# Performance work log

Measured on AMD Instinct MI355X. Metric: run time of the kernel, lower is better.

The kernel has to match this reference:

```python
import jax, jax.numpy as jnp
import numpy as np

N_NODES = 100000
N_EDGES = 3200000
IN_DIM = 128
OUT_DIM = 64
ITERS = 2


def setup_inputs() -> dict:
    key = jax.random.key(0)
    k1, k2, k3, k4, k5, k6 = jax.random.split(key, 6)
    feature = jax.random.normal(k1, (N_NODES, IN_DIM), dtype=jnp.float32)
    src = jax.random.randint(k2, (N_EDGES,), 0, N_NODES, dtype=jnp.int32)
    dst = jax.random.randint(k3, (N_EDGES,), 0, N_NODES, dtype=jnp.int32)
    # Kaiming-ish scaling for stability
    W_lin = jax.random.normal(k4, (IN_DIM, OUT_DIM), dtype=jnp.float32) / np.sqrt(IN_DIM)
    W_d1 = jax.random.normal(k5, (OUT_DIM, OUT_DIM), dtype=jnp.float32) / np.sqrt(OUT_DIM)
    W_d2 = jax.random.normal(k6, (OUT_DIM, OUT_DIM), dtype=jnp.float32) / np.sqrt(OUT_DIM)
    return {"feature": feature, "src": src, "dst": dst,
            "W_lin": W_lin, "W_d1": W_d1, "W_d2": W_d2}


def reference(feature, src, dst, W_lin, W_d1, W_d2):
    # u_i^0 = 0 ; u_i^j = tanh(linear(x_i) + dense(sum_{k in N(i)} u_k^{j-1}))
    base = feature @ W_lin                       # [N, OUT_DIM] (no bias)
    n = feature.shape[0]
    u = jnp.zeros((n, OUT_DIM), dtype=feature.dtype)
    for _ in range(ITERS):
        # copy_u + sum: message u[src] scattered-summed at dst
        m = jax.ops.segment_sum(u[src], dst, num_segments=n)   # [N, OUT_DIM]
        # Dense (2 layers, relu between, no bias): W_d2 @ relu(W_d1 @ m)
        h = jax.nn.relu(m @ W_d1) @ W_d2
        u = jnp.tanh(base + h)
    return u
```

## Files before the change

### kernel.cpp

```cpp
#include <hip/hip_runtime.h>
#include <math.h>

#define N_NODES 100000
#define N_EDGES 3200000
#define IN_DIM  128
#define OUT_DIM 64

#define BSHIFT   7
#define BNODES   128
#define NBUCKETS ((N_NODES + BNODES - 1) / BNODES)
#define NBINBLK  1024
#define CHUNK    (N_EDGES / NBINBLK)
#define SEGCAP   6144
#define MTILES   (N_NODES / 16)

typedef _Float16 half8 __attribute__((ext_vector_type(8)));
typedef float    f32x4 __attribute__((ext_vector_type(4)));

__device__ __forceinline__ int xcd_swz(int i) {
    return (i & 7) * (NBINBLK / 8) + (i >> 3);
}

__global__ __launch_bounds__(256) void gemm_base_tanh(
    const float* __restrict__ feature,
    const float* __restrict__ Wlin,
    float* __restrict__ base,
    _Float16* __restrict__ u1h)
{
    int lane = threadIdx.x & 63;
    int wid  = (blockIdx.x * 256 + threadIdx.x) >> 6;
    if (wid >= MTILES) return;

    int mrow = lane & 15;
    int kb   = lane >> 4;
    int k0   = kb * 8;

    half8 b[4][4];
#pragma unroll
    for (int s = 0; s < 4; ++s)
#pragma unroll
        for (int n = 0; n < 4; ++n)
#pragma unroll
            for (int j = 0; j < 8; ++j)
                b[s][n][j] = (_Float16)Wlin[(s * 32 + k0 + j) * OUT_DIM + n * 16 + mrow];

    int row = wid * 16 + mrow;
    const float4* fr = reinterpret_cast<const float4*>(feature + (size_t)row * IN_DIM);
    half8 a[4];
#pragma unroll
    for (int s = 0; s < 4; ++s) {
        float4 lo = fr[(s * 32 + k0) >> 2];
        float4 hi = fr[((s * 32 + k0) >> 2) + 1];
        a[s][0] = (_Float16)lo.x; a[s][1] = (_Float16)lo.y;
        a[s][2] = (_Float16)lo.z; a[s][3] = (_Float16)lo.w;
        a[s][4] = (_Float16)hi.x; a[s][5] = (_Float16)hi.y;
        a[s][6] = (_Float16)hi.z; a[s][7] = (_Float16)hi.w;
    }

    f32x4 acc[4];
#pragma unroll
    for (int n = 0; n < 4; ++n) acc[n] = (f32x4)0.f;

#pragma unroll
    for (int s = 0; s < 4; ++s)
#pragma unroll
        for (int n = 0; n < 4; ++n)
            acc[n] = __builtin_amdgcn_mfma_f32_16x16x32_f16(a[s], b[s][n], acc[n], 0, 0, 0);

#pragma unroll
    for (int n = 0; n < 4; ++n)
#pragma unroll
        for (int j = 0; j < 4; ++j) {
            int r = wid * 16 + kb * 4 + j;
            int c = n * 16 + mrow;
            float v = acc[n][j];
            base[(size_t)r * OUT_DIM + c] = v;
            u1h[(size_t)r * OUT_DIM + c] = (_Float16)tanhf(v);
        }
}

__global__ __launch_bounds__(256) void bin_hist(
    const int* __restrict__ dst, int* __restrict__ H)
{
    __shared__ int h[NBUCKETS];
    for (int k = threadIdx.x; k < NBUCKETS; k += 256) h[k] = 0;
    __syncthreads();

    int b = xcd_swz(blockIdx.x);
    int beg = b * CHUNK, end = beg + CHUNK;
    for (int i = beg + threadIdx.x; i < end; i += 256)
        atomicAdd(&h[dst[i] >> BSHIFT], 1);
    __syncthreads();

    for (int k = threadIdx.x; k < NBUCKETS; k += 256)
        H[(size_t)k * NBINBLK + b] = h[k];
}

__global__ __launch_bounds__(NBINBLK) void scan_local(
    int* __restrict__ H, int* __restrict__ Btot)
{
    __shared__ int s[NBINBLK];
    int k = blockIdx.x, t = threadIdx.x;
    int v = H[(size_t)k * NBINBLK + t];
    s[t] = v;
    __syncthreads();
#pragma unroll
    for (int off = 1; off < NBINBLK; off <<= 1) {
        int x = (t >= off) ? s[t - off] : 0;
        __syncthreads();
        s[t] += x;
        __syncthreads();
    }
    H[(size_t)k * NBINBLK + t] = s[t] - v;
    if (t == NBINBLK - 1) Btot[k] = s[t];
}

__global__ __launch_bounds__(1024) void scan_tot(int* __restrict__ Btot)
{
    __shared__ int s[1024];
    int t = threadIdx.x;
    int v = (t < NBUCKETS) ? Btot[t] : 0;
    s[t] = v;
    __syncthreads();
#pragma unroll
    for (int off = 1; off < 1024; off <<= 1) {
        int x = (t >= off) ? s[t - off] : 0;
        __syncthreads();
        s[t] += x;
        __syncthreads();
    }
    if (t < NBUCKETS) Btot[t] = s[t] - v;
}

__global__ __launch_bounds__(NBINBLK) void add_base(
    int* __restrict__ H, const int* __restrict__ Btot)
{
    int k = blockIdx.x, t = threadIdx.x;
    H[(size_t)k * NBINBLK + t] += Btot[k];
    if (k == 0 && t == 0) H[(size_t)NBUCKETS * NBINBLK] = N_EDGES;
}

__global__ __launch_bounds__(256) void bin_scatter(
    const int* __restrict__ src,
    const int* __restrict__ dst,
    const int* __restrict__ H,
    int* __restrict__ ebuf)
{
    __shared__ int cur[NBUCKETS];
    int b = xcd_swz(blockIdx.x);
    for (int k = threadIdx.x; k < NBUCKETS; k += 256)
        cur[k] = H[(size_t)k * NBINBLK + b];
    __syncthreads();

    int beg = b * CHUNK, end = beg + CHUNK;
    for (int i = beg + threadIdx.x; i < end; i += 256) {
        int d = dst[i];
        int k = d >> BSHIFT;
        int p = atomicAdd(&cur[k], 1);
        ebuf[p] = src[i] | ((d & (BNODES - 1)) << 17);
    }
}

__global__ __launch_bounds__(256) void bucket_sort(
    const int* __restrict__ H,
    int* __restrict__ ebuf,
    int* __restrict__ node_off)
{
    __shared__ int seg[SEGCAP];
    __shared__ int cnt[BNODES];
    __shared__ int off[BNODES];
    int k = blockIdx.x;
    int beg = H[(size_t)k * NBINBLK];
    int end = H[(size_t)(k + 1) * NBINBLK];
    int n = end - beg;

    for (int j = threadIdx.x; j < BNODES; j += 256) cnt[j] = 0;
    __syncthreads();

    for (int i = threadIdx.x; i < n; i += 256) {
        int v = ebuf[beg + i];
        seg[i] = v;
        atomicAdd(&cnt[v >> 17], 1);
    }
    __syncthreads();

    if (threadIdx.x == 0) {
        int node0 = k * BNODES;
        int nvalid = N_NODES - node0; if (nvalid > BNODES) nvalid = BNODES;
        int excl = 0;
        for (int j = 0; j < nvalid; ++j) {
            off[j] = excl;
            node_off[node0 + j] = beg + excl;
            excl += cnt[j];
        }
        if (k == NBUCKETS - 1) node_off[N_NODES] = end;
    }
    __syncthreads();

    for (int i = threadIdx.x; i < n; i += 256) {
        int v = seg[i];
        int p = atomicAdd(&off[v >> 17], 1);
        ebuf[beg + p] = v & 0x1FFFF;
    }
}

__global__ __launch_bounds__(256) void node_gather(
    const int* __restrict__ node_off,
    const int* __restrict__ csr,
    const half8* __restrict__ u1v,
    float* __restrict__ m)
{
    int wid = (blockIdx.x * 256 + threadIdx.x) >> 6;
    if (wid >= N_NODES) return;
    int lane = threadIdx.x & 63;
    int q = lane >> 3, c = lane & 7;

    int beg = node_off[wid];
    int end = node_off[wid + 1];
    int cnt = end - beg;
    int per = (cnt + 7) >> 3;
    int gb  = beg + q * per;
    int ge  = gb + per; if (ge > end) ge = end;

    float acc[8];
#pragma unroll
    for (int i = 0; i < 8; ++i) acc[i] = 0.f;

    int e = gb;
    for (; e + 4 <= ge; e += 4) {
        int s0 = csr[e];
        int s1 = csr[e + 1];
        int s2 = csr[e + 2];
        int s3 = csr[e + 3];
        half8 a = u1v[(size_t)s0 * 8 + c];
        half8 b = u1v[(size_t)s1 * 8 + c];
        half8 g = u1v[(size_t)s2 * 8 + c];
        half8 d = u1v[(size_t)s3 * 8 + c];
#pragma unroll
        for (int i = 0; i < 8; ++i)
            acc[i] += ((float)a[i] + (float)b[i]) + ((float)g[i] + (float)d[i]);
    }
    for (; e < ge; ++e) {
        half8 a = u1v[(size_t)csr[e] * 8 + c];
#pragma unroll
        for (int i = 0; i < 8; ++i) acc[i] += (float)a[i];
    }

#pragma unroll
    for (int i = 0; i < 8; ++i) {
        acc[i] += __shfl_xor(acc[i], 8);
        acc[i] += __shfl_xor(acc[i], 16);
        acc[i] += __shfl_xor(acc[i], 32);
    }

    if (q == 0) {
        float4* mr = reinterpret_cast<float4*>(m + (size_t)wid * OUT_DIM + c * 8);
        mr[0] = make_float4(acc[0], acc[1], acc[2], acc[3]);
        mr[1] = make_float4(acc[4], acc[5], acc[6], acc[7]);
    }
}

__global__ __launch_bounds__(256) void dense_tanh(
    const float* __restrict__ m,
    const float* __restrict__ W1,
    const float* __restrict__ W2,
    const float* __restrict__ base,
    float* __restrict__ out)
{
    __shared__ _Float16 tl[4][16][72];
    int lane = threadIdx.x & 63;
    int w    = threadIdx.x >> 6;
    int wid  = (blockIdx.x * 256 + threadIdx.x) >> 6;
    if (wid >= MTILES) return;

    int mrow = lane & 15;
    int kb   = lane >> 4;
    int k0   = kb * 8;

    half8 b1[2][4], b2[2][4];
#pragma unroll
    for (int s = 0; s < 2; ++s)
#pragma unroll
        for (int n = 0; n < 4; ++n)
#pragma unroll
            for (int j = 0; j < 8; ++j) {
                b1[s][n][j] = (_Float16)W1[(s * 32 + k0 + j) * 64 + n * 16 + mrow];
                b2[s][n][j] = (_Float16)W2[(s * 32 + k0 + j) * 64 + n * 16 + mrow];
            }

    int row = wid * 16 + mrow;
    const float4* mr = reinterpret_cast<const float4*>(m + (size_t)row * 64);
    half8 a[2];
#pragma unroll
    for (int s = 0; s < 2; ++s) {
        float4 lo = mr[(s * 32 + k0) >> 2];
        float4 hi = mr[((s * 32 + k0) >> 2) + 1];
        a[s][0] = (_Float16)lo.x; a[s][1] = (_Float16)lo.y;
        a[s][2] = (_Float16)lo.z; a[s][3] = (_Float16)lo.w;
        a[s][4] = (_Float16)hi.x; a[s][5] = (_Float16)hi.y;
        a[s][6] = (_Float16)hi.z; a[s][7] = (_Float16)hi.w;
    }

    f32x4 acc1[4];
#pragma unroll
    for (int n = 0; n < 4; ++n) acc1[n] = (f32x4)0.f;
#pragma unroll
    for (int s = 0; s < 2; ++s)
#pragma unroll
        for (int n = 0; n < 4; ++n)
            acc1[n] = __builtin_amdgcn_mfma_f32_16x16x32_f16(a[s], b1[s][n], acc1[n], 0, 0, 0);

#pragma unroll
    for (int n = 0; n < 4; ++n)
#pragma unroll
        for (int j = 0; j < 4; ++j)
            tl[w][kb * 4 + j][n * 16 + mrow] = (_Float16)fmaxf(acc1[n][j], 0.f);

    half8 a2[2];
#pragma unroll
    for (int s = 0; s < 2; ++s)
        a2[s] = *reinterpret_cast<const half8*>(&tl[w][mrow][s * 32 + k0]);

    f32x4 acc2[4];
#pragma unroll
    for (int n = 0; n < 4; ++n) acc2[n] = (f32x4)0.f;
#pragma unroll
    for (int s = 0; s < 2; ++s)
#pragma unroll
        for (int n = 0; n < 4; ++n)
            acc2[n] = __builtin_amdgcn_mfma_f32_16x16x32_f16(a2[s], b2[s][n], acc2[n], 0, 0, 0);

#pragma unroll
    for (int n = 0; n < 4; ++n)
#pragma unroll
        for (int j = 0; j < 4; ++j) {
            int r = wid * 16 + kb * 4 + j;
            int c = n * 16 + mrow;
            out[(size_t)r * 64 + c] = tanhf(base[(size_t)r * 64 + c] + acc2[n][j]);
        }
}

extern "C" void kernel_launch(void* const* d_in, const int* in_sizes, int n_in,
                              void* d_out, int out_size, void* d_ws, size_t ws_size,
                              hipStream_t stream)
{
    const float* feature = (const float*)d_in[0];
    const int*   src     = (const int*)d_in[1];
    const int*   dst     = (const int*)d_in[2];
    const float* W_lin   = (const float*)d_in[3];
    const float* W_d1    = (const float*)d_in[4];
    const float* W_d2    = (const float*)d_in[5];
    float* out = (float*)d_out;

    const size_t NODE_F = (size_t)N_NODES * OUT_DIM;

    float*    base     = (float*)d_ws;
    _Float16* u1h      = (_Float16*)(base + NODE_F);
    float*    m        = (float*)(u1h + NODE_F);
    int*      H        = (int*)(m + NODE_F);
    int*      Btot     = H + ((size_t)NBUCKETS * NBINBLK + 4);
    int*      node_off = Btot + (NBUCKETS + 4);
    int*      ebuf     = node_off + (N_NODES + 4);

    int gemm_blocks = (MTILES + 3) / 4;
    gemm_base_tanh<<<gemm_blocks, 256, 0, stream>>>(feature, W_lin, base, u1h);

    bin_hist  <<<NBINBLK, 256, 0, stream>>>(dst, H);
    scan_local<<<NBUCKETS, NBINBLK, 0, stream>>>(H, Btot);
    scan_tot  <<<1, 1024, 0, stream>>>(Btot);
    add_base  <<<NBUCKETS, NBINBLK, 0, stream>>>(H, Btot);
    bin_scatter<<<NBINBLK, 256, 0, stream>>>(src, dst, H, ebuf);
    bucket_sort<<<NBUCKETS, 256, 0, stream>>>(H, ebuf, node_off);

    int gather_blocks = (int)(((size_t)N_NODES * 64 + 255) / 256);
    node_gather<<<gather_blocks, 256, 0, stream>>>(
        node_off, ebuf, (const half8*)u1h, m);

    dense_tanh<<<gemm_blocks, 256, 0, stream>>>(m, W_d1, W_d2, base, out);
}
```

Before: 170.2 us.

## Fuse histogram into GEMM launch and fold bucket base offsets into consumers

Merges the edge-histogram kernel into the feature GEMM kernel as extra blocks of a single launch, so the two independent stages run concurrently. Removes the add_base pass by having bin_scatter add Btot when loading cursors and bucket_sort read bucket bounds directly from Btot. This saves two launches and a full read-modify-write over the histogram matrix. GEMM blocks now carry the histogram's shared memory allocation, which may affect occupancy.

```diff
diff --git a/kernel.cpp b/kernel.cpp
--- a/kernel.cpp
+++ b/kernel.cpp
@@ -13,6 +13,7 @@
 #define CHUNK    (N_EDGES / NBINBLK)
 #define SEGCAP   6144
 #define MTILES   (N_NODES / 16)
+#define GEMM_BLOCKS ((MTILES + 3) / 4)
 
 typedef _Float16 half8 __attribute__((ext_vector_type(8)));
 typedef float    f32x4 __attribute__((ext_vector_type(4)));
@@ -21,14 +22,33 @@
     return (i & 7) * (NBINBLK / 8) + (i >> 3);
 }
 
-__global__ __launch_bounds__(256) void gemm_base_tanh(
+__global__ __launch_bounds__(256) void fused_gemm_hist(
     const float* __restrict__ feature,
     const float* __restrict__ Wlin,
     float* __restrict__ base,
-    _Float16* __restrict__ u1h)
-{
+    _Float16* __restrict__ u1h,
+    const int* __restrict__ dst,
+    int* __restrict__ H)
+{
+    __shared__ int h[NBUCKETS];
+
+    if (blockIdx.x < NBINBLK) {
+        for (int k = threadIdx.x; k < NBUCKETS; k += 256) h[k] = 0;
+        __syncthreads();
+
+        int b = xcd_swz(blockIdx.x);
+        int beg = b * CHUNK, end = beg + CHUNK;
+        for (int i = beg + threadIdx.x; i < end; i += 256)
+            atomicAdd(&h[dst[i] >> BSHIFT], 1);
+        __syncthreads();
+
+        for (int k = threadIdx.x; k < NBUCKETS; k += 256)
+            H[(size_t)k * NBINBLK + b] = h[k];
+        return;
+    }
+
     int lane = threadIdx.x & 63;
-    int wid  = (blockIdx.x * 256 + threadIdx.x) >> 6;
+    int wid  = ((blockIdx.x - NBINBLK) * 256 + threadIdx.x) >> 6;
     if (wid >= MTILES) return;
 
     int mrow = lane & 15;
@@ -79,23 +99,6 @@
         }
 }
 
-__global__ __launch_bounds__(256) void bin_hist(
-    const int* __restrict__ dst, int* __restrict__ H)
-{
-    __shared__ int h[NBUCKETS];
-    for (int k = threadIdx.x; k < NBUCKETS; k += 256) h[k] = 0;
-    __syncthreads();
-
-    int b = xcd_swz(blockIdx.x);
-    int beg = b * CHUNK, end = beg + CHUNK;
-    for (int i = beg + threadIdx.x; i < end; i += 256)
-        atomicAdd(&h[dst[i] >> BSHIFT], 1);
-    __syncthreads();
-
-    for (int k = threadIdx.x; k < NBUCKETS; k += 256)
-        H[(size_t)k * NBINBLK + b] = h[k];
-}
-
 __global__ __launch_bounds__(NBINBLK) void scan_local(
     int* __restrict__ H, int* __restrict__ Btot)
 {
@@ -132,24 +135,17 @@
     if (t < NBUCKETS) Btot[t] = s[t] - v;
 }
 
-__global__ __launch_bounds__(NBINBLK) void add_base(
-    int* __restrict__ H, const int* __restrict__ Btot)
-{
-    int k = blockIdx.x, t = threadIdx.x;
-    H[(size_t)k * NBINBLK + t] += Btot[k];
-    if (k == 0 && t == 0) H[(size_t)NBUCKETS * NBINBLK] = N_EDGES;
-}
-
 __global__ __launch_bounds__(256) void bin_scatter(
     const int* __restrict__ src,
     const int* __restrict__ dst,
     const int* __restrict__ H,
+    const int* __restrict__ Btot,
     int* __restrict__ ebuf)
 {
     __shared__ int cur[NBUCKETS];
     int b = xcd_swz(blockIdx.x);
     for (int k = threadIdx.x; k < NBUCKETS; k += 256)
-        cur[k] = H[(size_t)k * NBINBLK + b];
+        cur[k] = H[(size_t)k * NBINBLK + b] + Btot[k];
     __syncthreads();
 
     int beg = b * CHUNK, end = beg + CHUNK;
@@ -162,7 +158,7 @@
 }
 
 __global__ __launch_bounds__(256) void bucket_sort(
-    const int* __restrict__ H,
+    const int* __restrict__ Btot,
     int* __restrict__ ebuf,
     int* __restrict__ node_off)
 {
@@ -170,8 +166,8 @@
     __shared__ int cnt[BNODES];
     __shared__ int off[BNODES];
     int k = blockIdx.x;
-    int beg = H[(size_t)k * NBINBLK];
-    int end = H[(size_t)(k + 1) * NBINBLK];
+    int beg = Btot[k];
+    int end = (k + 1 < NBUCKETS) ? Btot[k + 1] : N_EDGES;
     int n = end - beg;
 
     for (int j = threadIdx.x; j < BNODES; j += 256) cnt[j] = 0;
@@ -362,19 +358,17 @@
     int*      node_off = Btot + (NBUCKETS + 4);
     int*      ebuf     = node_off + (N_NODES + 4);
 
-    int gemm_blocks = (MTILES + 3) / 4;
-    gemm_base_tanh<<<gemm_blocks, 256, 0, stream>>>(feature, W_lin, base, u1h);
-
-    bin_hist  <<<NBINBLK, 256, 0, stream>>>(dst, H);
+    fused_gemm_hist<<<NBINBLK + GEMM_BLOCKS, 256, 0, stream>>>(
+        feature, W_lin, base, u1h, dst, H);
+
     scan_local<<<NBUCKETS, NBINBLK, 0, stream>>>(H, Btot);
     scan_tot  <<<1, 1024, 0, stream>>>(Btot);
-    add_base  <<<NBUCKETS, NBINBLK, 0, stream>>>(H, Btot);
-    bin_scatter<<<NBINBLK, 256, 0, stream>>>(src, dst, H, ebuf);
-    bucket_sort<<<NBUCKETS, 256, 0, stream>>>(H, ebuf, node_off);
+    bin_scatter<<<NBINBLK, 256, 0, stream>>>(src, dst, H, Btot, ebuf);
+    bucket_sort<<<NBUCKETS, 256, 0, stream>>>(Btot, ebuf, node_off);
 
     int gather_blocks = (int)(((size_t)N_NODES * 64 + 255) / 256);
     node_gather<<<gather_blocks, 256, 0, stream>>>(
         node_off, ebuf, (const half8*)u1h, m);
 
-    dense_tanh<<<gemm_blocks, 256, 0, stream>>>(m, W_d1, W_d2, base, out);
-}
+    dense_tanh<<<GEMM_BLOCKS, 256, 0, stream>>>(m, W_d1, W_d2, base, out);
+}
```

Measured after the change: 162.9 us. -4.3%, faster.
